# Kernel tuning notes

Hardware: AMD Instinct MI355X
Metric: run time of the kernel (lower is better)

Reference implementation:

```python
import jax, jax.numpy as jnp
import numpy as np

N_NODES = 48758  # hardcoded in the original DAN.forward
EPS_BN = 1e-5


def setup_inputs() -> dict:
    key = jax.random.key(0)
    ks = jax.random.split(key, 14)
    E, D, R, L, NI = 780000, 128, 4, 2, 10000
    sc = 1.0 / np.sqrt(D)
    inp = {
        "x": jax.random.normal(ks[0], (N_NODES, D), jnp.float32),
        "edge_index": jax.random.randint(ks[1], (2, E), 0, N_NODES),
        "idx": jax.random.randint(ks[2], (NI,), 0, N_NODES),
        "edge_type": jax.random.randint(ks[3], (E,), 0, R),
        "edge_weight": jax.random.uniform(ks[4], (E,), jnp.float32),
        # RiskGNN params
        "proj_w": jax.random.normal(ks[5], (D, D), jnp.float32) * sc,
        "proj_b": jax.random.normal(ks[6], (D,), jnp.float32) * 0.01,
        "bn_g": jnp.ones((D,), jnp.float32),
        "bn_b": jnp.zeros((D,), jnp.float32),
        # per-layer DAN params, stacked over L=2 layers (same dims)
        "win_w": jax.random.normal(ks[7], (L, D, D), jnp.float32) * sc,
        "win_b": jax.random.normal(ks[8], (L, D), jnp.float32) * 0.01,
        "wrel": jax.random.normal(ks[9], (L, R, D, D), jnp.float32) * sc,
        "out_w": jax.random.normal(ks[10], (L, D, D), jnp.float32) * sc,
        "out_b": jax.random.normal(ks[11], (L, D), jnp.float32) * 0.01,
    }
    return inp


def _dan_layer(h, edge_index, edge_type, rel_num, win_w, win_b, wrel, out_w, out_b):
    dst = edge_index[0]
    src = edge_index[1]
    x = h @ win_w + win_b                       # [N, D]
    x_j = x[src]                                # edge gather [E, D]
    # gcn_norm(add_self_loops=False): deg over col (=src axis edge_index[1])
    ones_e = jnp.ones(dst.shape[0], x.dtype)
    deg = jax.ops.segment_sum(ones_e, src, num_segments=N_NODES)
    dinv = jnp.where(deg > 0, jax.lax.rsqrt(jnp.maximum(deg, 1.0)), 0.0)
    norm_w = (dinv[dst] * dinv[src])[:, None]   # [E, 1]
    msg_gcn = jax.ops.segment_sum(x_j * norm_w, dst, num_segments=N_NODES)
    # per-relation masked matmul (unsorted grouped GEMM)
    res = jnp.zeros_like(x_j)
    for r in range(rel_num):
        res = jnp.where((edge_type == r)[:, None], x_j @ wrel[r], res)
    # segment softmax over edges grouped by dst, per channel
    seg_max = jax.ops.segment_max(res, dst, num_segments=N_NODES)
    ex = jnp.exp(res - seg_max[dst])
    denom = jax.ops.segment_sum(ex, dst, num_segments=N_NODES)
    weig = ex / denom[dst]
    msg = jax.ops.segment_sum(res * weig, dst, num_segments=N_NODES)
    out = (msg_gcn + 0.1 * jax.nn.relu(msg)) @ out_w + out_b
    return out


def reference(x, edge_weight, proj_w, proj_b, bn_g, bn_b, win_w, win_b, wrel,
              out_w, out_b, edge_index, edge_type, idx):
    rel_num = wrel.shape[1]
    n_layer = win_w.shape[0]
    h = x @ proj_w + proj_b
    # BatchNorm1d (training-mode batch stats, biased var)
    mu = jnp.mean(h, axis=0)
    var = jnp.mean((h - mu) ** 2, axis=0)
    h = (h - mu) * jax.lax.rsqrt(var + EPS_BN) * bn_g + bn_b
    h = jax.nn.relu(h)
    for i in range(n_layer):
        h = _dan_layer(h, edge_index, edge_type, rel_num,
                       win_w[i], win_b[i], wrel[i], out_w[i], out_b[i])
    h = jax.nn.gelu(h, approximate=False)  # dropout is identity at eval
    return h[idx]
```

## Files before the change

### kernel.cpp

```cpp
#include <hip/hip_runtime.h>
#include <hip/hip_bf16.h>
#include <math.h>

#define D 128
#define DD (128 * 128)
#define RS 640
#define CAPB 4608

typedef __attribute__((ext_vector_type(8))) short short8;
typedef __attribute__((ext_vector_type(4))) float f32x4;

__device__ __forceinline__ float bf2f(unsigned short u) {
    union { unsigned int i; float f; } x; x.i = ((unsigned int)u) << 16; return x.f;
}
__device__ __forceinline__ unsigned short f2bf(float f) {
    unsigned int i = __float_as_uint(f);
    unsigned int r = (i + 0x7FFFu + ((i >> 16) & 1u)) >> 16;
    return (unsigned short)r;
}

__device__ __forceinline__ int vote_flag(const unsigned short* __restrict__ x) {
    __shared__ int bad_s;
    if (threadIdx.x == 0) bad_s = 0;
    __syncthreads();
    unsigned int e = (x[threadIdx.x] >> 7) & 0xFFu;
    unsigned long long b = __ballot(e < 100u || e > 140u);
    if ((threadIdx.x & 63) == 0) atomicAdd(&bad_s, __popcll(b));
    __syncthreads();
    return bad_s > 48 ? 1 : 0;
}

__global__ __launch_bounds__(256) void k_stage1(
    const void* __restrict__ xin, unsigned short* __restrict__ xb, int n4, int nbx, int nbw,
    const void* s0, const void* s1, const void* s2, const void* s3,
    const void* s4, const void* s5, const void* s6, const void* s7, const void* s8,
    int o1, int o2, int o3, int o4, int o5, int o6, int o7, int o8,
    int total, unsigned short* __restrict__ wdst,
    const int* __restrict__ ei, const int* __restrict__ et, int E,
    unsigned int* __restrict__ cd_g, unsigned int* __restrict__ cs_g,
    uint2* __restrict__ ebuck, unsigned short* __restrict__ sbuck)
{
    int bx = blockIdx.x, t = threadIdx.x;
    if (bx < nbx) {
        int fl = vote_flag((const unsigned short*)xin);
        int i = bx * 256 + t;
        if (i >= n4) return;
        if (fl) {
            float4 v = ((const float4*)xin)[i];
            uint2 o;
            o.x = (unsigned int)f2bf(v.x) | ((unsigned int)f2bf(v.y) << 16);
            o.y = (unsigned int)f2bf(v.z) | ((unsigned int)f2bf(v.w) << 16);
            ((uint2*)xb)[i] = o;
        } else {
            ((uint2*)xb)[i] = ((const uint2*)xin)[i];
        }
    } else if (bx < nbx + nbw) {
        int fl = vote_flag((const unsigned short*)xin);
        int i = (bx - nbx) * 256 + t;
        if (i >= total) return;
        const void* src; int base;
        if      (i < o1) { src = s0; base = 0;  }
        else if (i < o2) { src = s1; base = o1; }
        else if (i < o3) { src = s2; base = o2; }
        else if (i < o4) { src = s3; base = o3; }
        else if (i < o5) { src = s4; base = o4; }
        else if (i < o6) { src = s5; base = o5; }
        else if (i < o7) { src = s6; base = o6; }
        else if (i < o8) { src = s7; base = o7; }
        else             { src = s8; base = o8; }
        int li = i - base;
        wdst[i] = fl ? f2bf(((const float*)src)[li]) : ((const unsigned short*)src)[li];
    } else {
        __shared__ unsigned int hd[256], hs[256];
        int b = bx - nbx - nbw;
        hd[t] = 0u; hs[t] = 0u;
        unsigned int d8[8], sp8[8];
        __syncthreads();
        int base = b * 2048;
        #pragma unroll
        for (int i = 0; i < 8; ++i) {
            int e = base + t + i * 256;
            if (e < E) {
                unsigned int d = (unsigned int)ei[e];
                unsigned int s = (unsigned int)ei[E + e];
                unsigned int tt = (unsigned int)et[e];
                d8[i] = d; sp8[i] = s | (tt << 16);
                atomicAdd(&hd[d >> 8], 1u);
                atomicAdd(&hs[s >> 8], 1u);
            } else d8[i] = 0xFFFFFFFFu;
        }
        __syncthreads();
        hd[t] = atomicAdd(&cd_g[t], hd[t]);
        hs[t] = atomicAdd(&cs_g[t], hs[t]);
        __syncthreads();
        #pragma unroll
        for (int i = 0; i < 8; ++i) {
            if (d8[i] != 0xFFFFFFFFu) {
                unsigned int bk = d8[i] >> 8;
                unsigned int pos = atomicAdd(&hd[bk], 1u);
                if (pos < (unsigned)CAPB) ebuck[(size_t)bk * CAPB + pos] = make_uint2(d8[i], sp8[i]);
                unsigned int s = sp8[i] & 0xFFFFu;
                unsigned int bk2 = s >> 8;
                unsigned int pos2 = atomicAdd(&hs[bk2], 1u);
                if (pos2 < (unsigned)CAPB) sbuck[(size_t)bk2 * CAPB + pos2] = (unsigned short)s;
            }
        }
    }
}

__device__ __forceinline__ void gemm_core(
    const unsigned short* __restrict__ A, const unsigned short* __restrict__ W,
    unsigned short* As, unsigned short* Wt, f32x4 (&acc)[2][8])
{
    int t = threadIdx.x;
    #pragma unroll
    for (int i = 0; i < 8; ++i) {
        int ch = t + i * 256;
        int row = ch >> 4;
        int kc  = ch & 15;
        uint4 v = *((const uint4*)(A + (size_t)row * D + kc * 8));
        *((uint4*)&As[row * 128 + (kc ^ (row & 15)) * 8]) = v;
    }
    #pragma unroll
    for (int i = 0; i < 8; ++i) {
        int ch = t + i * 256;
        int k  = ch >> 4;
        int n0 = (ch & 15) * 8;
        uint4 v = *((const uint4*)(W + k * D + n0));
        const unsigned short* pv = (const unsigned short*)&v;
        int kc = k >> 3, ko = k & 7;
        #pragma unroll
        for (int j = 0; j < 8; ++j) {
            int n = n0 + j;
            Wt[n * 128 + ((kc ^ (n & 15)) * 8) + ko] = pv[j];
        }
    }
    __syncthreads();
    int wave = t >> 6, lane = t & 63, quad = lane >> 4, l16 = lane & 15;
    int rowbase = wave * 32;
    #pragma unroll
    for (int a = 0; a < 2; ++a)
        #pragma unroll
        for (int b = 0; b < 8; ++b) acc[a][b] = (f32x4){0.f, 0.f, 0.f, 0.f};
    #pragma unroll
    for (int ks = 0; ks < 4; ++ks) {
        int chunk = ks * 4 + quad;
        short8 af[2], bf[8];
        #pragma unroll
        for (int rt = 0; rt < 2; ++rt) {
            int r = rowbase + rt * 16 + l16;
            af[rt] = *((const short8*)&As[r * 128 + (chunk ^ (r & 15)) * 8]);
        }
        #pragma unroll
        for (int ct = 0; ct < 8; ++ct) {
            int n = ct * 16 + l16;
            bf[ct] = *((const short8*)&Wt[n * 128 + (chunk ^ (n & 15)) * 8]);
        }
        #pragma unroll
        for (int rt = 0; rt < 2; ++rt)
            #pragma unroll
            for (int ct = 0; ct < 8; ++ct)
                acc[rt][ct] = __builtin_amdgcn_mfma_f32_16x16x32_bf16(af[rt], bf[ct], acc[rt][ct], 0, 0, 0);
    }
}

__device__ __forceinline__ void store_transposed(f32x4 (&acc)[2][8], unsigned short* dst)
{
    int t = threadIdx.x;
    int wave = t >> 6, lane = t & 63, quad = lane >> 4, l16 = lane & 15;
    int rowbase = wave * 32;
    #pragma unroll
    for (int rt = 0; rt < 2; ++rt) {
        #pragma unroll
        for (int ct = 0; ct < 8; ++ct) {
            int n = ct * 16 + l16;
            #pragma unroll
            for (int r = 0; r < 4; ++r) {
                int k = rowbase + rt * 16 + quad * 4 + r;
                dst[n * 128 + (((k >> 3) ^ (n & 15)) * 8) + (k & 7)] = f2bf(acc[rt][ct][r]);
            }
        }
    }
}

__global__ __launch_bounds__(256) void k_stage2(
    const unsigned int* __restrict__ cd_g, const uint2* __restrict__ ebuck,
    unsigned int* __restrict__ rp, unsigned int* __restrict__ pckd,
    const unsigned int* __restrict__ cs_g, const unsigned short* __restrict__ sbuck,
    float* __restrict__ dinv, int N, int NB,
    const unsigned short* __restrict__ wbase, unsigned short* __restrict__ bc,
    unsigned short* __restrict__ wtg, unsigned short* __restrict__ wraw,
    unsigned short* __restrict__ bxl1, int o4, int o5, int o6, int o7, int o8)
{
    __shared__ __align__(16) char pool[65536];
    int bx = blockIdx.x, t = threadIdx.x;
    if (bx < NB) {
        uint2* ebuf = (uint2*)pool;
        unsigned int* bins = (unsigned int*)(pool + CAPB * 8);
        unsigned int* gsum = bins + 1024;
        unsigned int* csc  = gsum + 256;
        int b = bx;
        unsigned int cvt_ = (t < NB) ? min(cd_g[t], (unsigned)CAPB) : 0u;
        csc[t] = cvt_;
        __syncthreads();
        for (int off = 1; off < 256; off <<= 1) {
            unsigned int v = csc[t];
            unsigned int a = (t >= off) ? csc[t - off] : 0u;
            __syncthreads();
            csc[t] = v + a;
            __syncthreads();
        }
        unsigned int cnt = min(cd_g[b], (unsigned)CAPB);
        unsigned int beg = csc[b] - cnt;
        #pragma unroll
        for (int j = 0; j < 4; ++j) bins[t + j * 256] = 0u;
        __syncthreads();
        for (unsigned int i = t; i < cnt; i += 256) {
            uint2 v = ebuck[(size_t)b * CAPB + i];
            ebuf[i] = v;
            atomicAdd(&bins[((v.x & 255u) << 2) | ((v.y >> 16) & 3u)], 1u);
        }
        __syncthreads();
        unsigned int b0 = bins[4 * t], b1 = bins[4 * t + 1], b2 = bins[4 * t + 2], b3 = bins[4 * t + 3];
        unsigned int s4 = b0 + b1 + b2 + b3;
        gsum[t] = s4;
        __syncthreads();
        for (int off = 1; off < 256; off <<= 1) {
            unsigned int v = gsum[t];
            unsigned int a = (t >= off) ? gsum[t - off] : 0u;
            __syncthreads();
            gsum[t] = v + a;
            __syncthreads();
        }
        unsigned int base0 = gsum[t] - s4;
        bins[4 * t]     = beg + base0;
        bins[4 * t + 1] = beg + base0 + b0;
        bins[4 * t + 2] = beg + base0 + b0 + b1;
        bins[4 * t + 3] = beg + base0 + b0 + b1 + b2;
        int n = (b << 8) + t;
        if (n <= N) rp[n] = beg + base0;
        __syncthreads();
        for (unsigned int i = t; i < cnt; i += 256) {
            uint2 v = ebuf[i];
            unsigned int key = ((v.x & 255u) << 2) | ((v.y >> 16) & 3u);
            unsigned int pos = atomicAdd(&bins[key], 1u);
            pckd[pos] = v.y;
        }
    } else if (bx < 2 * NB) {
        unsigned int* bins = (unsigned int*)pool;
        int b = bx - NB;
        unsigned int cnt = min(cs_g[b], (unsigned)CAPB);
        bins[t] = 0u;
        __syncthreads();
        for (unsigned int i = t; i < cnt; i += 256)
            atomicAdd(&bins[sbuck[(size_t)b * CAPB + i] & 255u], 1u);
        __syncthreads();
        int n = (b << 8) + t;
        if (n < N) {
            unsigned int dg = bins[t];
            dinv[n] = dg ? rsqrtf((float)dg) : 0.f;
        }
    } else if (bx < 2 * NB + 4) {
        int r = bx - 2 * NB;
        const unsigned short* A = wbase + o4;
        const unsigned short* W = wbase + o6 + (size_t)r * DD;
        f32x4 acc[2][8];
        gemm_core(A, W, (unsigned short*)pool, (unsigned short*)pool + DD, acc);
        store_transposed(acc, wtg + (size_t)(3 + r) * DD);
        const unsigned short* b_in0 = wbase + o5;
        if (t < 128) {
            float s = 0.f;
            for (int k = 0; k < 128; ++k)
                s += bf2f(b_in0[k]) * bf2f(W[k * D + t]);
            bc[r * D + t] = f2bf(s);
        }
    } else if (bx == 2 * NB + 4) {
        const unsigned short* A = wbase + o7;
        const unsigned short* W = wbase + o4 + DD;
        f32x4 acc[2][8];
        gemm_core(A, W, (unsigned short*)pool, (unsigned short*)pool + DD, acc);
        store_transposed(acc, wtg + (size_t)2 * DD);
        int wave = t >> 6, lane = t & 63, quad = lane >> 4, l16 = lane & 15;
        int rowbase = wave * 32;
        #pragma unroll
        for (int rt = 0; rt < 2; ++rt)
            #pragma unroll
            for (int ct = 0; ct < 8; ++ct) {
                int col = ct * 16 + l16;
                #pragma unroll
                for (int r = 0; r < 4; ++r) {
                    int row = rowbase + rt * 16 + quad * 4 + r;
                    wraw[row * 128 + col] = f2bf(acc[rt][ct][r]);
                }
            }
        const unsigned short* b_out0 = wbase + o8;
        const unsigned short* b_in1  = wbase + o5 + D;
        if (t < 128) {
            float s = bf2f(b_in1[t]);
            for (int k = 0; k < 128; ++k)
                s += bf2f(b_out0[k]) * bf2f(W[k * D + t]);
            bxl1[t] = f2bf(s);
        }
    } else {
        int pb = bx - 2 * NB - 5;
        int mi = pb >> 3, sub = pb & 7;
        const unsigned short* src;
        int m;
        if (mi == 0)      { src = wbase;            m = 0;  }
        else if (mi == 1) { src = wbase + o4;       m = 1;  }
        else              { src = wbase + o7 + DD;  m = 12; }
        int c = sub * 256 + t;
        int n = c >> 4, kc = c & 15;
        unsigned short tmp[8];
        #pragma unroll
        for (int ko = 0; ko < 8; ++ko) tmp[ko] = src[(kc * 8 + ko) * 128 + n];
        *((uint4*)(wtg + (size_t)m * DD + n * 128 + ((kc ^ (n & 15)) * 8))) = *(uint4*)tmp;
    }
}

__device__ __forceinline__ void load_afrag(
    const unsigned short* __restrict__ A, int M, int blockRow, short8 (&af)[2][4])
{
    int t = threadIdx.x;
    int wave = t >> 6, lane = t & 63, quad = lane >> 4, l16 = lane & 15;
    int rowbase = blockRow + wave * 32;
    int r0 = min(rowbase + l16, M - 1);
    int r1 = min(rowbase + 16 + l16, M - 1);
    const unsigned short* a0 = A + (size_t)r0 * D;
    const unsigned short* a1 = A + (size_t)r1 * D;
    #pragma unroll
    for (int ks = 0; ks < 4; ++ks) {
        int chunk = ks * 4 + quad;
        af[0][ks] = *((const short8*)(a0 + chunk * 8));
        af[1][ks] = *((const short8*)(a1 + chunk * 8));
    }
}

__device__ __forceinline__ void mfma_slice(
    const unsigned short* Wt, short8 (&af)[2][4], f32x4 (&acc)[2][8])
{
    int lane = threadIdx.x & 63, quad = lane >> 4, l16 = lane & 15;
    #pragma unroll
    for (int a = 0; a < 2; ++a)
        #pragma unroll
        for (int b = 0; b < 8; ++b) acc[a][b] = (f32x4){0.f, 0.f, 0.f, 0.f};
    #pragma unroll
    for (int ks = 0; ks < 4; ++ks) {
        int chunk = ks * 4 + quad;
        short8 bf[8];
        #pragma unroll
        for (int ct = 0; ct < 8; ++ct)
            bf[ct] = *((const short8*)&Wt[(ct * 16 + l16) * 128 + ((chunk ^ l16) * 8)]);
        #pragma unroll
        for (int rt = 0; rt < 2; ++rt)
            #pragma unroll
            for (int ct = 0; ct < 8; ++ct)
                acc[rt][ct] = __builtin_amdgcn_mfma_f32_16x16x32_bf16(af[rt][ks], bf[ct], acc[rt][ct], 0, 0, 0);
    }
}

__device__ __forceinline__ void gemm_core_fast(
    const unsigned short* __restrict__ A, const unsigned short* __restrict__ Wt_g,
    int M, int blockRow, unsigned short* Wt, f32x4 (&acc)[2][8])
{
    int t = threadIdx.x;
    #pragma unroll
    for (int i = 0; i < 8; ++i)
        ((uint4*)Wt)[t + i * 256] = ((const uint4*)Wt_g)[t + i * 256];
    short8 af[2][4];
    load_afrag(A, M, blockRow, af);
    __syncthreads();
    mfma_slice(Wt, af, acc);
}

__global__ __launch_bounds__(256) void gemm_proj(
    const unsigned short* __restrict__ A, const unsigned short* __restrict__ Wt_g,
    const unsigned short* __restrict__ bias, unsigned short* __restrict__ C,
    int M, float* __restrict__ psum, float* __restrict__ psq, int gb,
    const unsigned short* __restrict__ wraw, const unsigned short* __restrict__ wbase,
    const unsigned short* __restrict__ bxl1, unsigned short* __restrict__ bc,
    unsigned short* __restrict__ wtg, int o6)
{
    __shared__ __align__(16) char pool[2 * DD * 2 + 4096];
    int t = threadIdx.x;
    if (blockIdx.x >= gb) {
        int r = blockIdx.x - gb;
        const unsigned short* W = wbase + o6 + (size_t)(4 + r) * DD;
        f32x4 acc[2][8];
        gemm_core(wraw, W, (unsigned short*)pool, (unsigned short*)pool + DD, acc);
        store_transposed(acc, wtg + (size_t)(7 + r) * DD);
        if (t < 128) {
            float s = 0.f;
            for (int k = 0; k < 128; ++k)
                s += bf2f(bxl1[k]) * bf2f(W[k * D + t]);
            bc[(4 + r) * D + t] = f2bf(s);
        }
        return;
    }
    unsigned short* Wt = (unsigned short*)pool;
    float* smS = (float*)(pool + 2 * DD * 2);
    float* smQ = smS + 512;
    f32x4 acc[2][8];
    int blockRow = blockIdx.x * 128;
    gemm_core_fast(A, Wt_g, M, blockRow, Wt, acc);
    int wave = t >> 6, lane = t & 63, quad = lane >> 4, l16 = lane & 15;
    int rowbase = wave * 32;
    #pragma unroll
    for (int ct = 0; ct < 8; ++ct) {
        int col = ct * 16 + l16;
        float bv = bf2f(bias[col]);
        float ps = 0.f, pq = 0.f;
        #pragma unroll
        for (int rt = 0; rt < 2; ++rt) {
            #pragma unroll
            for (int r = 0; r < 4; ++r) {
                int grow = blockRow + rowbase + rt * 16 + quad * 4 + r;
                if (grow < M) {
                    float v = acc[rt][ct][r] + bv;
                    C[(size_t)grow * D + col] = f2bf(v);
                    ps += v; pq += v * v;
                }
            }
        }
        ps += __shfl_xor(ps, 16, 64); ps += __shfl_xor(ps, 32, 64);
        pq += __shfl_xor(pq, 16, 64); pq += __shfl_xor(pq, 32, 64);
        if (quad == 0) { smS[wave * 128 + col] = ps; smQ[wave * 128 + col] = pq; }
    }
    __syncthreads();
    if (t < 128) {
        psum[blockIdx.x * 128 + t] = smS[t] + smS[128 + t] + smS[256 + t] + smS[384 + t];
        psq[blockIdx.x * 128 + t]  = smQ[t] + smQ[128 + t] + smQ[256 + t] + smQ[384 + t];
    }
}

__global__ __launch_bounds__(256) void k_bnstats(
    const float* __restrict__ psum, const float* __restrict__ psq,
    int nb, int N, const unsigned short* __restrict__ g,
    const unsigned short* __restrict__ b,
    float* __restrict__ scale, float* __restrict__ shift)
{
    int col = blockIdx.x, t = threadIdx.x;
    float s = 0.f, q = 0.f;
    for (int i = t; i < nb; i += 256) {
        s += psum[i * 128 + col];
        q += psq[i * 128 + col];
    }
    #pragma unroll
    for (int o = 32; o >= 1; o >>= 1) {
        s += __shfl_xor(s, o, 64);
        q += __shfl_xor(q, o, 64);
    }
    __shared__ float sS[4], sQ[4];
    if ((t & 63) == 0) { sS[t >> 6] = s; sQ[t >> 6] = q; }
    __syncthreads();
    if (t == 0) {
        s = sS[0] + sS[1] + sS[2] + sS[3];
        q = sQ[0] + sQ[1] + sQ[2] + sQ[3];
        float inv = 1.f / (float)N;
        float mean = s * inv;
        float var = fmaxf(q * inv - mean * mean, 0.f);
        float sc = rsqrtf(var + 1e-5f) * bf2f(g[col]);
        scale[col] = sc;
        shift[col] = bf2f(b[col]) - mean * sc;
    }
}

__global__ __launch_bounds__(256) void gemm_fused(
    const unsigned short* __restrict__ h, const unsigned short* __restrict__ wtg,
    const unsigned short* __restrict__ b_in_l, const unsigned short* __restrict__ bc_l,
    unsigned char* __restrict__ xy8, const float* __restrict__ dinv,
    const float* __restrict__ bnsc, const float* __restrict__ bnsh, int M, int l)
{
    __shared__ unsigned short Wt[DD];
    f32x4 acc[2][8];
    int slice = blockIdx.y;
    int m = (slice == 0) ? (1 + l) : (3 + l * 4 + slice - 1);
    int blockRow = blockIdx.x * 128;
    int t = threadIdx.x;
    const unsigned short* Wt_g = wtg + (size_t)m * DD;
    #pragma unroll
    for (int i = 0; i < 8; ++i)
        ((uint4*)Wt)[t + i * 256] = ((const uint4*)Wt_g)[t + i * 256];
    short8 af[2][4];
    load_afrag(h, M, blockRow, af);
    if (bnsc) {
        int quad = (t & 63) >> 4;
        #pragma unroll
        for (int rt = 0; rt < 2; ++rt)
            #pragma unroll
            for (int ks = 0; ks < 4; ++ks) {
                int ch0 = (ks * 4 + quad) * 8;
                unsigned short* p = (unsigned short*)&af[rt][ks];
                #pragma unroll
                for (int j = 0; j < 8; ++j) {
                    float f = bf2f(p[j]);
                    f = fmaxf(fmaf(f, bnsc[ch0 + j], bnsh[ch0 + j]), 0.f);
                    p[j] = f2bf(f);
                }
            }
    }
    __syncthreads();
    mfma_slice(Wt, af, acc);

    int wave = t >> 6, lane = t & 63, quad = lane >> 4, l16 = lane & 15;
    int rowbase = wave * 32;
    int boff = (slice == 0) ? 0 : (128 + (slice - 1) * 128);
    #pragma unroll
    for (int rt = 0; rt < 2; ++rt) {
        float dv[4];
        if (slice == 0) {
            #pragma unroll
            for (int r = 0; r < 4; ++r) {
                int grow = min(blockRow + rowbase + rt * 16 + quad * 4 + r, M - 1);
                dv[r] = dinv[grow];
            }
        }
        #pragma unroll
        for (int ct = 0; ct < 8; ++ct) {
            int col = ct * 16 + l16;
            float bv = (slice == 0) ? bf2f(b_in_l[col]) : bf2f(bc_l[(slice - 1) * D + col]);
            #pragma unroll
            for (int r = 0; r < 4; ++r) {
                int grow = blockRow + rowbase + rt * 16 + quad * 4 + r;
                if (grow < M) {
                    float v = acc[rt][ct][r] + bv;
                    if (slice == 0) v *= dv[r];
                    int p = __builtin_amdgcn_cvt_pk_fp8_f32(v, v, 0, false);
                    xy8[(size_t)grow * RS + boff + col] = (unsigned char)(p & 0xFF);
                }
            }
        }
    }
}

__global__ __launch_bounds__(256) void gemm_out(
    const unsigned short* __restrict__ zg, const unsigned short* __restrict__ Wt_g,
    const unsigned short* __restrict__ bias, void* __restrict__ out,
    int M, const unsigned short* __restrict__ xprobe)
{
    int fl = vote_flag(xprobe);
    __shared__ unsigned short Wt[DD];
    f32x4 acc[2][8];
    int blockRow = blockIdx.x * 128;
    gemm_core_fast(zg, Wt_g, M, blockRow, Wt, acc);
    int t = threadIdx.x;
    int wave = t >> 6, lane = t & 63, quad = lane >> 4, l16 = lane & 15;
    int rowbase = wave * 32;
    #pragma unroll
    for (int rt = 0; rt < 2; ++rt) {
        #pragma unroll
        for (int ct = 0; ct < 8; ++ct) {
            int col = ct * 16 + l16;
            float bv = bf2f(bias[col]);
            #pragma unroll
            for (int r = 0; r < 4; ++r) {
                int grow = blockRow + rowbase + rt * 16 + quad * 4 + r;
                if (grow < M) {
                    float v = acc[rt][ct][r] + bv;
                    float gl = 0.5f * v * (1.f + erff(v * 0.70710678118654752f));
                    size_t o = (size_t)grow * D + col;
                    if (fl) ((float*)out)[o] = gl;
                    else    ((unsigned short*)out)[o] = f2bf(gl);
                }
            }
        }
    }
}

__device__ __forceinline__ void acc_edge2(uint2 xv, uint2 yv, float vm,
                                          float* g, float* dd, float* ss) {
    const unsigned int* xw = (const unsigned int*)&xv;
    const unsigned int* yw = (const unsigned int*)&yv;
    #pragma unroll
    for (int w = 0; w < 2; ++w) {
        auto xlo = __builtin_amdgcn_cvt_pk_f32_fp8(xw[w], false);
        auto xhi = __builtin_amdgcn_cvt_pk_f32_fp8(xw[w], true);
        auto ylo = __builtin_amdgcn_cvt_pk_f32_fp8(yw[w], false);
        auto yhi = __builtin_amdgcn_cvt_pk_f32_fp8(yw[w], true);
        float vx[4] = {xlo[0], xlo[1], xhi[0], xhi[1]};
        float vy[4] = {ylo[0], ylo[1], yhi[0], yhi[1]};
        int j = 4 * w;
        #pragma unroll
        for (int i = 0; i < 4; ++i) {
            g[j + i] = fmaf(vx[i], vm, g[j + i]);
            float e = __expf(vy[i]);
            dd[j + i] = fmaf(e, vm, dd[j + i]);
            ss[j + i] = fmaf(vy[i] * e, vm, ss[j + i]);
        }
    }
}

__global__ __launch_bounds__(256) void k_edge(
    const unsigned int* __restrict__ rp, const unsigned int* __restrict__ packed,
    const unsigned char* __restrict__ xy8, const float* __restrict__ dinv,
    unsigned short* __restrict__ zout, int NN, const int* __restrict__ nodes)
{
    int lane = threadIdx.x & 63;
    int slot = blockIdx.x * 4 + (threadIdx.x >> 6);
    if (slot >= NN) return;
    int node = nodes ? nodes[slot] : slot;
    node = __builtin_amdgcn_readfirstlane(node);
    unsigned int beg = rp[node], end = rp[node + 1];
    int eg = lane >> 4;
    int cb = (lane & 15) * 8;
    float g[8], dd[8], ss[8];
    #pragma unroll
    for (int j = 0; j < 8; ++j) { g[j] = 0.f; dd[j] = 0.f; ss[j] = 0.f; }

    for (unsigned int e0 = beg; e0 < end; e0 += 16) {
        unsigned int pk[4];
        float vm[4];
        #pragma unroll
        for (int u = 0; u < 4; ++u) {
            unsigned int e = e0 + u * 4 + (unsigned int)eg;
            vm[u] = (e < end) ? 1.f : 0.f;
            pk[u] = packed[(e < end) ? e : beg];
        }
        uint2 xv[4], yv[4];
        #pragma unroll
        for (int u = 0; u < 4; ++u) {
            unsigned int s = pk[u] & 0xFFFFu;
            unsigned int tt = (pk[u] >> 16) & 3u;
            const unsigned char* bp = xy8 + (size_t)s * RS;
            xv[u] = *((const uint2*)(bp + cb));
            yv[u] = *((const uint2*)(bp + 128 + tt * 128 + cb));
        }
        #pragma unroll
        for (int u = 0; u < 4; ++u) acc_edge2(xv[u], yv[u], vm[u], g, dd, ss);
    }

    #pragma unroll
    for (int j = 0; j < 8; ++j) {
        g[j]  += __shfl_xor(g[j], 16, 64);  g[j]  += __shfl_xor(g[j], 32, 64);
        dd[j] += __shfl_xor(dd[j], 16, 64); dd[j] += __shfl_xor(dd[j], 32, 64);
        ss[j] += __shfl_xor(ss[j], 16, 64); ss[j] += __shfl_xor(ss[j], 32, 64);
    }
    if (eg == 0) {
        float dn = dinv[node];
        unsigned int o[4];
        #pragma unroll
        for (int w = 0; w < 4; ++w) {
            int j0 = w * 2, j1 = w * 2 + 1;
            float m0 = (dd[j0] > 0.f) ? ss[j0] / dd[j0] : 0.f;
            float m1 = (dd[j1] > 0.f) ? ss[j1] / dd[j1] : 0.f;
            float z0 = fmaf(g[j0], dn, 0.1f * fmaxf(m0, 0.f));
            float z1 = fmaf(g[j1], dn, 0.1f * fmaxf(m1, 0.f));
            o[w] = (unsigned int)f2bf(z0) | ((unsigned int)f2bf(z1) << 16);
        }
        *((uint4*)(zout + (size_t)slot * D + cb)) = *(uint4*)o;
    }
}

extern "C" void kernel_launch(void* const* d_in, const int* in_sizes, int n_in,
                              void* d_out, int out_size, void* d_ws, size_t ws_size,
                              hipStream_t stream)
{
    const int* ei  = (const int*)d_in[1];
    const int* idx = (const int*)d_in[2];
    const int* et  = (const int*)d_in[3];
    const unsigned short* xprobe = (const unsigned short*)d_in[0];

    int N  = in_sizes[0] / D;
    int E  = in_sizes[1] / 2;
    int NI = in_sizes[2];
    int L  = in_sizes[9] / (D * D);
    int R  = in_sizes[11] / (L * D * D);

    int NB = (N + 255) >> 8;
    int BA = (E + 2047) / 2048;

    char* ws = (char*)d_ws;
    size_t off = 0;
    auto alloc = [&](size_t bytes) -> char* {
        char* p = ws + off;
        off += (bytes + 255) & ~(size_t)255;
        return p;
    };
    unsigned short* h    = (unsigned short*)alloc((size_t)N * D * 2);
    unsigned char*  xy8  = (unsigned char*)alloc((size_t)N * RS);
    unsigned short* z    = (unsigned short*)alloc((size_t)N * D * 2);
    unsigned short* xb   = (unsigned short*)alloc((size_t)N * D * 2);
    unsigned short* zg   = (unsigned short*)alloc((size_t)NI * D * 2);
    float*          dinv = (float*)alloc((size_t)N * 4);
    unsigned int*   rp   = (unsigned int*)alloc((size_t)(N + 1) * 4);
    unsigned int*   pckd = (unsigned int*)alloc((size_t)E * 4);
    int gb  = (N + 127) / 128;
    float*          psum = (float*)alloc((size_t)gb * 128 * 4);
    float*          psq  = (float*)alloc((size_t)gb * 128 * 4);
    float*          bscale = (float*)alloc(128 * 4);
    float*          bshift = (float*)alloc(128 * 4);
    unsigned int*   cursors = (unsigned int*)alloc(512 * 4);
    unsigned int*   cd_g = cursors;
    unsigned int*   cs_g = cursors + 256;
    uint2*          ebuck = (uint2*)xy8;
    unsigned short* sbuck = (unsigned short*)z;
    int o1 = D * D;
    int o2 = o1 + D;
    int o3 = o2 + D;
    int o4 = o3 + D;
    int o5 = o4 + L * D * D;
    int o6 = o5 + L * D;
    int o7 = o6 + L * R * D * D;
    int o8 = o7 + L * D * D;
    int wt = o8 + L * D;
    unsigned short* wbase  = (unsigned short*)alloc((size_t)wt * 2);
    unsigned short* b_proj = wbase + o1;
    unsigned short* g_bn   = wbase + o2;
    unsigned short* b_bn   = wbase + o3;
    unsigned short* b_in   = wbase + o5;
    unsigned short* b_out  = wbase + o8;
    unsigned short* bc     = (unsigned short*)alloc((size_t)L * R * D * 2);
    unsigned short* wtg    = (unsigned short*)alloc((size_t)13 * DD * 2);
    unsigned short* wraw   = (unsigned short*)alloc((size_t)DD * 2);
    unsigned short* bxl1   = (unsigned short*)alloc((size_t)D * 2);
    (void)ws_size; (void)n_in; (void)out_size;

    int gb2 = (NI + 127) / 128;
    int nb4 = (N + 3) / 4;
    int ni4 = (NI + 3) / 4;
    int n4 = N * D / 4;
    int nbx = (n4 + 255) / 256;
    int nbw = (wt + 255) / 256;

    hipMemsetAsync(cursors, 0, 512 * 4, stream);

    k_stage1<<<nbx + nbw + BA, 256, 0, stream>>>(
        d_in[0], xb, n4, nbx, nbw,
        d_in[5], d_in[6], d_in[7], d_in[8], d_in[9], d_in[10], d_in[11], d_in[12], d_in[13],
        o1, o2, o3, o4, o5, o6, o7, o8, wt, wbase,
        ei, et, E, cd_g, cs_g, ebuck, sbuck);

    k_stage2<<<2 * NB + 5 + 24, 256, 0, stream>>>(
        cd_g, ebuck, rp, pckd, cs_g, sbuck, dinv, N, NB,
        wbase, bc, wtg, wraw, bxl1, o4, o5, o6, o7, o8);

    gemm_proj<<<gb + R, 256, 0, stream>>>(xb, wtg, b_proj, h, N, psum, psq, gb,
                                          wraw, wbase, bxl1, bc, wtg, o6);
    k_bnstats<<<128, 256, 0, stream>>>(psum, psq, gb, N, g_bn, b_bn, bscale, bshift);

    gemm_fused<<<dim3(gb, 1 + R), 256, 0, stream>>>(h, wtg, b_in, bc, xy8, dinv, bscale, bshift, N, 0);
    k_edge<<<nb4, 256, 0, stream>>>(rp, pckd, xy8, dinv, z, N, nullptr);

    gemm_fused<<<dim3(gb, 1 + R), 256, 0, stream>>>(z, wtg, bxl1, bc + R * D, xy8, dinv, nullptr, nullptr, N, 1);
    k_edge<<<ni4, 256, 0, stream>>>(rp, pckd, xy8, dinv, zg, NI, idx);

    gemm_out<<<gb2, 256, 0, stream>>>(zg, wtg + (size_t)12 * DD, b_out + D, d_out, NI, xprobe);
}
```

Measured before the change: 312.1 us.

## Interleave x and per-relation y fp8 rows so each edge gathers one contiguous vector

The fp8 node table now stores, for each relation, the projected x value next to the relation-transformed y value, giving four 256-byte blocks per row. Each gemm_fused block computes both the x GEMM and one relation GEMM, so x is recomputed R times and the write traffic grows. In exchange, the edge kernel fetches one 16-byte load per edge instead of two separate 8-byte gathers and processes 8 edges per iteration instead of 16. The goal is fewer, wider random gathers in the edge-aggregation kernel.

```diff
diff --git a/kernel.cpp b/kernel.cpp
--- a/kernel.cpp
+++ b/kernel.cpp
@@ -4,7 +4,7 @@
 
 #define D 128
 #define DD (128 * 128)
-#define RS 640
+#define RS 1024
 #define CAPB 4608
 
 typedef __attribute__((ext_vector_type(8))) short short8;
@@ -472,24 +472,21 @@
     const float* __restrict__ bnsc, const float* __restrict__ bnsh, int M, int l)
 {
     __shared__ unsigned short Wt[DD];
-    f32x4 acc[2][8];
-    int slice = blockIdx.y;
-    int m = (slice == 0) ? (1 + l) : (3 + l * 4 + slice - 1);
+    int r_ = blockIdx.y;
+    int m_x = 1 + l;
+    int m_y = 3 + l * 4 + r_;
     int blockRow = blockIdx.x * 128;
     int t = threadIdx.x;
-    const unsigned short* Wt_g = wtg + (size_t)m * DD;
-    #pragma unroll
-    for (int i = 0; i < 8; ++i)
-        ((uint4*)Wt)[t + i * 256] = ((const uint4*)Wt_g)[t + i * 256];
+
     short8 af[2][4];
     load_afrag(h, M, blockRow, af);
     if (bnsc) {
-        int quad = (t & 63) >> 4;
+        int quad_ = (t & 63) >> 4;
         #pragma unroll
         for (int rt = 0; rt < 2; ++rt)
             #pragma unroll
             for (int ks = 0; ks < 4; ++ks) {
-                int ch0 = (ks * 4 + quad) * 8;
+                int ch0 = (ks * 4 + quad_) * 8;
                 unsigned short* p = (unsigned short*)&af[rt][ks];
                 #pragma unroll
                 for (int j = 0; j < 8; ++j) {
@@ -499,34 +496,51 @@
                 }
             }
     }
+
+    f32x4 acc_x[2][8];
+    {
+        const unsigned short* Wt_g = wtg + (size_t)m_x * DD;
+        #pragma unroll
+        for (int i = 0; i < 8; ++i)
+            ((uint4*)Wt)[t + i * 256] = ((const uint4*)Wt_g)[t + i * 256];
+        __syncthreads();
+        mfma_slice(Wt, af, acc_x);
+    }
     __syncthreads();
-    mfma_slice(Wt, af, acc);
+    f32x4 acc_y[2][8];
+    {
+        const unsigned short* Wt_g = wtg + (size_t)m_y * DD;
+        #pragma unroll
+        for (int i = 0; i < 8; ++i)
+            ((uint4*)Wt)[t + i * 256] = ((const uint4*)Wt_g)[t + i * 256];
+        __syncthreads();
+        mfma_slice(Wt, af, acc_y);
+    }
 
     int wave = t >> 6, lane = t & 63, quad = lane >> 4, l16 = lane & 15;
     int rowbase = wave * 32;
-    int boff = (slice == 0) ? 0 : (128 + (slice - 1) * 128);
+    int boff = r_ * 256;
     #pragma unroll
     for (int rt = 0; rt < 2; ++rt) {
         float dv[4];
-        if (slice == 0) {
-            #pragma unroll
-            for (int r = 0; r < 4; ++r) {
-                int grow = min(blockRow + rowbase + rt * 16 + quad * 4 + r, M - 1);
-                dv[r] = dinv[grow];
-            }
+        #pragma unroll
+        for (int r = 0; r < 4; ++r) {
+            int grow = min(blockRow + rowbase + rt * 16 + quad * 4 + r, M - 1);
+            dv[r] = dinv[grow];
         }
         #pragma unroll
         for (int ct = 0; ct < 8; ++ct) {
             int col = ct * 16 + l16;
-            float bv = (slice == 0) ? bf2f(b_in_l[col]) : bf2f(bc_l[(slice - 1) * D + col]);
+            float bvx = bf2f(b_in_l[col]);
+            float bvy = bf2f(bc_l[r_ * D + col]);
             #pragma unroll
             for (int r = 0; r < 4; ++r) {
                 int grow = blockRow + rowbase + rt * 16 + quad * 4 + r;
                 if (grow < M) {
-                    float v = acc[rt][ct][r] + bv;
-                    if (slice == 0) v *= dv[r];
-                    int p = __builtin_amdgcn_cvt_pk_fp8_f32(v, v, 0, false);
-                    xy8[(size_t)grow * RS + boff + col] = (unsigned char)(p & 0xFF);
+                    float xv = (acc_x[rt][ct][r] + bvx) * dv[r];
+                    float yv = acc_y[rt][ct][r] + bvy;
+                    int p = __builtin_amdgcn_cvt_pk_fp8_f32(xv, yv, 0, false);
+                    *((unsigned short*)(xy8 + (size_t)grow * RS + boff + col * 2)) = (unsigned short)(p & 0xFFFF);
                 }
             }
         }
@@ -567,26 +581,20 @@
     }
 }
 
-__device__ __forceinline__ void acc_edge2(uint2 xv, uint2 yv, float vm,
-                                          float* g, float* dd, float* ss) {
-    const unsigned int* xw = (const unsigned int*)&xv;
-    const unsigned int* yw = (const unsigned int*)&yv;
-    #pragma unroll
-    for (int w = 0; w < 2; ++w) {
-        auto xlo = __builtin_amdgcn_cvt_pk_f32_fp8(xw[w], false);
-        auto xhi = __builtin_amdgcn_cvt_pk_f32_fp8(xw[w], true);
-        auto ylo = __builtin_amdgcn_cvt_pk_f32_fp8(yw[w], false);
-        auto yhi = __builtin_amdgcn_cvt_pk_f32_fp8(yw[w], true);
-        float vx[4] = {xlo[0], xlo[1], xhi[0], xhi[1]};
-        float vy[4] = {ylo[0], ylo[1], yhi[0], yhi[1]};
-        int j = 4 * w;
-        #pragma unroll
-        for (int i = 0; i < 4; ++i) {
-            g[j + i] = fmaf(vx[i], vm, g[j + i]);
-            float e = __expf(vy[i]);
-            dd[j + i] = fmaf(e, vm, dd[j + i]);
-            ss[j + i] = fmaf(vy[i] * e, vm, ss[j + i]);
-        }
+__device__ __forceinline__ void acc_edge4(uint4 v, float vm, float* g, float* dd, float* ss) {
+    const unsigned int* w = (const unsigned int*)&v;
+    #pragma unroll
+    for (int j = 0; j < 4; ++j) {
+        auto lo = __builtin_amdgcn_cvt_pk_f32_fp8(w[j], false);
+        auto hi = __builtin_amdgcn_cvt_pk_f32_fp8(w[j], true);
+        int c0 = 2 * j, c1 = 2 * j + 1;
+        g[c0] = fmaf(lo[0], vm, g[c0]);
+        g[c1] = fmaf(hi[0], vm, g[c1]);
+        float e0 = __expf(lo[1]), e1 = __expf(hi[1]);
+        dd[c0] = fmaf(e0, vm, dd[c0]);
+        dd[c1] = fmaf(e1, vm, dd[c1]);
+        ss[c0] = fmaf(lo[1] * e0, vm, ss[c0]);
+        ss[c1] = fmaf(hi[1] * e1, vm, ss[c1]);
     }
 }
 
@@ -602,31 +610,24 @@
     node = __builtin_amdgcn_readfirstlane(node);
     unsigned int beg = rp[node], end = rp[node + 1];
     int eg = lane >> 4;
-    int cb = (lane & 15) * 8;
+    int cb2 = (lane & 15) * 16;
     float g[8], dd[8], ss[8];
     #pragma unroll
     for (int j = 0; j < 8; ++j) { g[j] = 0.f; dd[j] = 0.f; ss[j] = 0.f; }
 
-    for (unsigned int e0 = beg; e0 < end; e0 += 16) {
-        unsigned int pk[4];
-        float vm[4];
-        #pragma unroll
-        for (int u = 0; u < 4; ++u) {
-            unsigned int e = e0 + u * 4 + (unsigned int)eg;
-            vm[u] = (e < end) ? 1.f : 0.f;
-            pk[u] = packed[(e < end) ? e : beg];
-        }
-        uint2 xv[4], yv[4];
-        #pragma unroll
-        for (int u = 0; u < 4; ++u) {
-            unsigned int s = pk[u] & 0xFFFFu;
-            unsigned int tt = (pk[u] >> 16) & 3u;
-            const unsigned char* bp = xy8 + (size_t)s * RS;
-            xv[u] = *((const uint2*)(bp + cb));
-            yv[u] = *((const uint2*)(bp + 128 + tt * 128 + cb));
-        }
-        #pragma unroll
-        for (int u = 0; u < 4; ++u) acc_edge2(xv[u], yv[u], vm[u], g, dd, ss);
+    for (unsigned int e0 = beg; e0 < end; e0 += 8) {
+        unsigned int eA = e0 + (unsigned int)eg;
+        unsigned int eB = eA + 4u;
+        float vmA = (eA < end) ? 1.f : 0.f;
+        float vmB = (eB < end) ? 1.f : 0.f;
+        unsigned int pA = packed[(eA < end) ? eA : beg];
+        unsigned int pB = packed[(eB < end) ? eB : beg];
+        unsigned int sA = pA & 0xFFFFu, tA = (pA >> 16) & 3u;
+        unsigned int sB = pB & 0xFFFFu, tB = (pB >> 16) & 3u;
+        uint4 vA = *((const uint4*)(xy8 + (size_t)sA * RS + tA * 256 + cb2));
+        uint4 vB = *((const uint4*)(xy8 + (size_t)sB * RS + tB * 256 + cb2));
+        acc_edge4(vA, vmA, g, dd, ss);
+        acc_edge4(vB, vmB, g, dd, ss);
     }
 
     #pragma unroll
@@ -647,7 +648,7 @@
             float z1 = fmaf(g[j1], dn, 0.1f * fmaxf(m1, 0.f));
             o[w] = (unsigned int)f2bf(z0) | ((unsigned int)f2bf(z1) << 16);
         }
-        *((uint4*)(zout + (size_t)slot * D + cb)) = *(uint4*)o;
+        *((uint4*)(zout + (size_t)slot * D + (lane & 15) * 8)) = *(uint4*)o;
     }
 }
 
@@ -738,10 +739,10 @@
                                           wraw, wbase, bxl1, bc, wtg, o6);
     k_bnstats<<<128, 256, 0, stream>>>(psum, psq, gb, N, g_bn, b_bn, bscale, bshift);
 
-    gemm_fused<<<dim3(gb, 1 + R), 256, 0, stream>>>(h, wtg, b_in, bc, xy8, dinv, bscale, bshift, N, 0);
+    gemm_fused<<<dim3(gb, R), 256, 0, stream>>>(h, wtg, b_in, bc, xy8, dinv, bscale, bshift, N, 0);
     k_edge<<<nb4, 256, 0, stream>>>(rp, pckd, xy8, dinv, z, N, nullptr);
 
-    gemm_fused<<<dim3(gb, 1 + R), 256, 0, stream>>>(z, wtg, bxl1, bc + R * D, xy8, dinv, nullptr, nullptr, N, 1);
+    gemm_fused<<<dim3(gb, R), 256, 0, stream>>>(z, wtg, bxl1, bc + R * D, xy8, dinv, nullptr, nullptr, N, 1);
     k_edge<<<ni4, 256, 0, stream>>>(rp, pckd, xy8, dinv, zg, NI, idx);
 
     gemm_out<<<gb2, 256, 0, stream>>>(zg, wtg + (size_t)12 * DD, b_out + D, d_out, NI, xprobe);
```

After: 344.7 us. 1.1x slower.
